# Performance work log

Measured on AMD Instinct MI355X. Metric: run time of the kernel, lower is better.

## Reference

```python
import jax, jax.numpy as jnp
import numpy as np
from jax import lax

B, C, H, W = 4, 64, 256, 256
CH = C // 2  # attention hidden channels


def conv2d_same(x, w, b):
    # x: [B,Ci,H,W], w: [Co,Ci,kh,kw]
    y = lax.conv_general_dilated(x, w, (1, 1), 'SAME',
                                 dimension_numbers=('NCHW', 'OIHW', 'NCHW'))
    return y + b[None, :, None, None]


def conv1x1(x, w):
    # w: [Co,Ci]
    return jnp.einsum('oi,bihw->bohw', w, x)


def irnn_scan(x, w, b, axis, reverse):
    """Directional IRNN: h_t = relu(x_t + w_c * h_{t-1} + b_c), per channel.
    axis: 2 (rows/H) or 3 (cols/W). reverse=True scans from the far edge
    (e.g. bottom-to-top for 'up', right-to-left for 'left')."""
    xs = jnp.moveaxis(x, axis, 0)            # [L, B, C, rest]
    wb = w[None, :, None]                    # broadcast over [B, C, rest]
    bb = b[None, :, None]

    def step(h, xt):
        h = jax.nn.relu(xt + wb * h + bb)
        return h, h

    h0 = jnp.zeros_like(xs[0])
    _, ys = lax.scan(step, h0, xs, reverse=reverse)
    return jnp.moveaxis(ys, 0, axis)


def setup_inputs() -> dict:
    key = jax.random.key(0)
    ks = jax.random.split(key, 16)
    d = {}
    d['x'] = jax.random.normal(ks[0], (B, C, H, W), dtype=jnp.float32)
    # conv_in: 1x1, no bias
    d['w_in'] = jax.random.normal(ks[1], (C, C), dtype=jnp.float32) * 0.05
    # IRNN depthwise 1x1 weights (init alpha=1.0 in torch) + biases
    for i, name in enumerate(['up', 'right', 'down', 'left']):
        d['w_' + name] = jnp.ones((C,), dtype=jnp.float32)
        d['b_' + name] = jax.random.normal(ks[2 + i], (C,), dtype=jnp.float32) * 0.01
    # convD2: 1x1, 4C -> C, no bias
    d['wD2'] = jax.random.normal(ks[6], (C, 4 * C), dtype=jnp.float32) * 0.01
    # attention layers
    d['a1_w'] = jax.random.normal(ks[7], (CH, C, 3, 3), dtype=jnp.float32) * 0.05
    d['a1_b'] = jnp.zeros((CH,), dtype=jnp.float32)
    d['a2_w'] = jax.random.normal(ks[8], (CH, CH, 3, 3), dtype=jnp.float32) * 0.05
    d['a2_b'] = jnp.zeros((CH,), dtype=jnp.float32)
    d['a3_w'] = jax.random.normal(ks[9], (1, CH), dtype=jnp.float32) * 0.05
    d['a3_b'] = jnp.zeros((1,), dtype=jnp.float32)
    return d


def reference(x, w_in, w_up, b_up, w_right, b_right, w_down, b_down,
              w_left, b_left, wD2, a1_w, a1_b, a2_w, a2_b, a3_w, a3_b):
    out = conv1x1(x, w_in)
    # four directional spatial IRNN scans
    top_up = irnn_scan(out, w_up, b_up, axis=2, reverse=True)     # bottom->top
    top_right = irnn_scan(out, w_right, b_right, axis=3, reverse=False)  # left->right
    top_down = irnn_scan(out, w_down, b_down, axis=2, reverse=False)     # top->bottom
    top_left = irnn_scan(out, w_left, b_left, axis=3, reverse=True)      # right->left
    cat = jnp.concatenate([top_up, top_right, top_down, top_left], axis=1)  # [B,4C,H,W]
    out = jax.nn.relu(conv1x1(cat, wD2))
    # attention gate
    a = jax.nn.relu(conv2d_same(out, a1_w, a1_b))
    a = jax.nn.relu(conv2d_same(a, a2_w, a2_b))
    a = conv1x1(a, a3_w) + a3_b[None, :, None, None]
    weight = jax.nn.sigmoid(a)                # [B,1,H,W]
    return jax.nn.relu(x * weight)
```

## Files before the change

kernel.cpp:

```cpp
#include <hip/hip_runtime.h>
#include <hip/hip_bf16.h>

#define HWSZ  65536

typedef unsigned short ushort_t;
typedef unsigned int   uint_t;
typedef __attribute__((ext_vector_type(8))) _Float16 half8;
typedef __attribute__((ext_vector_type(4))) float f32x4;

static __device__ __forceinline__ void gl_lds16(const void* g, void* l) {
    __builtin_amdgcn_global_load_lds(
        (const __attribute__((address_space(1))) unsigned int*)g,
        (__attribute__((address_space(3))) unsigned int*)l, 16, 0, 0);
}

__global__ __launch_bounds__(256) void k1_mfma(
    const float* __restrict__ x, const float* __restrict__ w_in,
    _Float16* __restrict__ out0)
{
    __shared__ float xs[64][64];
    int b   = blockIdx.x >> 10;
    int hw0 = (blockIdx.x & 1023) << 6;
    const float* xb = x + ((size_t)b * 64) * HWSZ + hw0;
    int wave = threadIdx.x >> 6, lane = threadIdx.x & 63;
    int n16 = lane & 15, quad = lane >> 4;

    for (int idx = threadIdx.x; idx < 1024; idx += 256) {
        int i = idx >> 4, p4 = (idx & 15) << 2;
        *(float4*)&xs[i][p4] = *(const float4*)(xb + (size_t)i * HWSZ + p4);
    }

    half8 Bh[2], Bl[2];
#pragma unroll
    for (int s = 0; s < 2; s++) {
        const float* wp = w_in + (wave * 16 + n16) * 64 + s * 32 + quad * 8;
#pragma unroll
        for (int j = 0; j < 8; j++) {
            float v = wp[j];
            _Float16 h = (_Float16)v;
            float r = v - (float)h;
            Bh[s][j] = h; Bl[s][j] = (_Float16)r;
        }
    }
    __syncthreads();

    f32x4 acc[4] = {};
#pragma unroll
    for (int j = 0; j < 4; j++) {
#pragma unroll
        for (int s = 0; s < 2; s++) {
            half8 Ah, Al;
#pragma unroll
            for (int jj = 0; jj < 8; jj++) {
                float v = xs[s * 32 + quad * 8 + jj][j * 16 + n16];
                _Float16 h = (_Float16)v;
                float r = v - (float)h;
                Ah[jj] = h; Al[jj] = (_Float16)r;
            }
            acc[j] = __builtin_amdgcn_mfma_f32_16x16x32_f16(Ah, Bh[s], acc[j], 0, 0, 0);
            acc[j] = __builtin_amdgcn_mfma_f32_16x16x32_f16(Al, Bh[s], acc[j], 0, 0, 0);
            acc[j] = __builtin_amdgcn_mfma_f32_16x16x32_f16(Ah, Bl[s], acc[j], 0, 0, 0);
        }
    }
    _Float16* ob = out0 + ((size_t)b * HWSZ + hw0) * 64 + wave * 16;
#pragma unroll
    for (int j = 0; j < 4; j++)
#pragma unroll
        for (int r = 0; r < 4; r++) {
            int px = j * 16 + quad * 4 + r;
            ob[(size_t)px * 64 + n16] = (_Float16)acc[j][r];
        }
}

__global__ __launch_bounds__(256) void k2_scan(
    const _Float16* __restrict__ out0,
    const float* __restrict__ w_up, const float* __restrict__ b_up,
    const float* __restrict__ w_rt, const float* __restrict__ b_rt,
    const float* __restrict__ w_dn, const float* __restrict__ b_dn,
    const float* __restrict__ w_lf, const float* __restrict__ b_lf,
    _Float16* __restrict__ cat)
{
    int c = threadIdx.x & 63;
    int q = threadIdx.x >> 6;
    bool vert = blockIdx.x < 256;
    int bid = blockIdx.x & 255;
    int b = bid >> 6, g = bid & 63;
    int line = g * 4 + q;
    size_t base = (size_t)b * HWSZ;

    float w0v, b0v, w1v, b1v; int coff0, coff1;
    if (vert) { w0v = w_dn[c]; b0v = b_dn[c]; coff0 = 128;
                w1v = w_up[c]; b1v = b_up[c]; coff1 = 0; }
    else      { w0v = w_rt[c]; b0v = b_rt[c]; coff0 = 64;
                w1v = w_lf[c]; b1v = b_lf[c]; coff1 = 192; }

#pragma unroll
    for (int pass = 0; pass < 2; pass++) {
        float wv = pass ? w1v : w0v, bv = pass ? b1v : b0v;
        int coff = pass ? coff1 : coff0;
        float h = 0.f;
        for (int k0 = 0; k0 < 256; k0 += 8) {
            float v[8];
#pragma unroll
            for (int jx = 0; jx < 8; jx++) {
                int i = pass ? 255 - (k0 + jx) : (k0 + jx);
                size_t pix = vert ? (base + i * 256 + line) : (base + line * 256 + i);
                v[jx] = (float)out0[pix * 64 + c];
            }
#pragma unroll
            for (int jx = 0; jx < 8; jx++) {
                int i = pass ? 255 - (k0 + jx) : (k0 + jx);
                size_t pix = vert ? (base + i * 256 + line) : (base + line * 256 + i);
                h = fmaxf(0.f, v[jx] + wv * h + bv);
                cat[pix * 256 + coff + c] = (_Float16)h;
            }
        }
    }
}

__global__ __launch_bounds__(256) void packall(
    const float* __restrict__ wD2, const float* __restrict__ a1w,
    const float* __restrict__ a2w,
    _Float16* __restrict__ wf, _Float16* __restrict__ p1,
    _Float16* __restrict__ p2)
{
    int i = blockIdx.x * 256 + threadIdx.x;
    if (i < 16384) {
        wf[i] = (_Float16)wD2[i];
        return;
    }
    int k = i - 16384;
    if (k < 18432) {
        int j = k & 7, lane = (k >> 3) & 63, st = k >> 9;
        int s = st >> 1, t = st & 1;
        int oc = t * 16 + (lane & 15);
        int gk = s * 32 + (lane >> 4) * 8 + j;
        int dydx = gk >> 6, ic = gk & 63;
        p1[k] = (_Float16)a1w[((oc * 64 + ic) * 3 + dydx / 3) * 3 + dydx % 3];
    } else if (k < 27648) {
        int e = k - 18432;
        int j = e & 7, lane = (e >> 3) & 63, st = e >> 9;
        int s = st >> 1, t = st & 1;
        int oc = t * 16 + (lane & 15);
        int gk = s * 32 + (lane >> 4) * 8 + j;
        int dydx = gk >> 5, ic = gk & 31;
        p2[e] = (_Float16)a2w[((oc * 32 + ic) * 3 + dydx / 3) * 3 + dydx % 3];
    }
}

__global__ __launch_bounds__(256) void k3_mfma(
    const _Float16* __restrict__ cat, const _Float16* __restrict__ wf,
    _Float16* __restrict__ out3)
{
    __shared__ _Float16 As[64 * 256];
    int wave = threadIdx.x >> 6, lane = threadIdx.x & 63;
    int n16 = lane & 15, quad = lane >> 4;
    size_t p0 = (size_t)blockIdx.x * 64;

    half8 B[8];
#pragma unroll
    for (int s = 0; s < 8; s++)
        B[s] = *(const half8*)(wf + (size_t)(wave * 16 + n16) * 256 + s * 32 + quad * 8);

#pragma unroll
    for (int it = 0; it < 8; it++) {
        int px = wave * 16 + it * 2 + (lane >> 5);
        int pu = lane & 31;
        int lu = pu ^ (px & 7);
        const _Float16* gp = cat + ((p0 + px) << 8) + lu * 8;
        _Float16* lp = As + wave * 4096 + it * 512;
        gl_lds16(gp, lp);
    }
    __syncthreads();

    f32x4 acc[4] = {};
#pragma unroll
    for (int j = 0; j < 4; j++) {
        int px = j * 16 + n16;
        const _Float16* lrow = As + px * 256;
        int x7 = px & 7;
#pragma unroll
        for (int s = 0; s < 8; s++) {
            int phys = (s * 4 + quad) ^ x7;
            half8 a = *(const half8*)(lrow + phys * 8);
            acc[j] = __builtin_amdgcn_mfma_f32_16x16x32_f16(a, B[s], acc[j], 0, 0, 0);
        }
    }

#pragma unroll
    for (int j = 0; j < 4; j++)
#pragma unroll
        for (int r = 0; r < 4; r++) {
            size_t op = (p0 + j * 16 + quad * 4 + r) * 64 + wave * 16 + n16;
            out3[op] = (_Float16)fmaxf(acc[j][r], 0.f);
        }
}

template <int IC>
__global__ __launch_bounds__(256) void convmfma(
    const _Float16* __restrict__ in, const _Float16* __restrict__ pb,
    const float* __restrict__ bias, _Float16* __restrict__ oh)
{
    constexpr int UPX = IC / 8;
    constexpr int KST = IC / 32;
    constexpr int PPS = 64 / UPX;
    __shared__ _Float16 Ls[6 * 66 * IC];

    int wave = threadIdx.x >> 6, lane = threadIdx.x & 63;
    int n16 = lane & 15, quad = lane >> 4;
    int bid = blockIdx.x;
    int bb  = bid >> 8;
    int hh0 = ((bid >> 2) & 63) << 2;
    int w0  = (bid & 3) << 6;
    const _Float16* ib = in + (size_t)bb * HWSZ * IC;

#pragma unroll
    for (int it = 0; it < (6 * UPX) / 4; it++) {
        int q   = it * 4 + wave;
        int r   = q / UPX, seg = q % UPX;
        int gh  = hh0 - 1 + r;
        int pxr = seg * PPS + lane / UPX;
        int pu  = lane % UPX;
        int px_lin = r * 66 + 1 + pxr;
        int lu  = (UPX == 8) ? (pu ^ (px_lin & 7)) : pu;
        _Float16* lp = Ls + (size_t)(r * 66 + 1 + seg * PPS) * IC;
        if ((unsigned)gh < 256u) {
            const _Float16* gp = ib + ((size_t)(gh * 256 + w0 + pxr)) * IC + lu * 8;
            gl_lds16(gp, lp);
        } else {
            half8 z = {};
            *(half8*)(lp + (size_t)lane * 8) = z;
        }
    }
    if (threadIdx.x < 12 * UPX) {
        int pu = threadIdx.x % UPX;
        int ph = threadIdx.x / UPX;
        int r = ph >> 1, side = ph & 1;
        int col = side ? 65 : 0;
        int gh = hh0 - 1 + r;
        int gw = w0 - 1 + side * 65;
        int px_lin = r * 66 + col;
        int lu = (UPX == 8) ? (pu ^ (px_lin & 7)) : pu;
        half8 v = {};
        if ((unsigned)gh < 256u && (unsigned)gw < 256u)
            v = *(const half8*)(ib + ((size_t)(gh * 256 + gw)) * IC + lu * 8);
        *(half8*)(Ls + (size_t)px_lin * IC + pu * 8) = v;
    }
    __syncthreads();

    f32x4 acc[4][2] = {};
#pragma unroll
    for (int dydx = 0; dydx < 9; dydx++) {
        int dy = dydx / 3, dx = dydx % 3;
        int r_lds = wave + dy;
#pragma unroll
        for (int kst = 0; kst < KST; kst++) {
            int s = dydx * KST + kst;
            half8 B0 = *(const half8*)(pb + (size_t)((s * 2 + 0) * 64 + lane) * 8);
            half8 B1 = *(const half8*)(pb + (size_t)((s * 2 + 1) * 64 + lane) * 8);
            int u = kst * 4 + quad;
#pragma unroll
            for (int j = 0; j < 4; j++) {
                int px_lin = r_lds * 66 + j * 16 + n16 + dx;
                int phys = (UPX == 8) ? (u ^ (px_lin & 7)) : u;
                half8 A = *(const half8*)(Ls + (size_t)px_lin * IC + phys * 8);
                acc[j][0] = __builtin_amdgcn_mfma_f32_16x16x32_f16(A, B0, acc[j][0], 0, 0, 0);
                acc[j][1] = __builtin_amdgcn_mfma_f32_16x16x32_f16(A, B1, acc[j][1], 0, 0, 0);
            }
        }
    }

    int hh = hh0 + wave;
#pragma unroll
    for (int t = 0; t < 2; t++) {
        float bv = bias[t * 16 + n16];
#pragma unroll
        for (int j = 0; j < 4; j++)
#pragma unroll
            for (int r = 0; r < 4; r++) {
                int wp = w0 + j * 16 + quad * 4 + r;
                size_t op = ((size_t)bb * HWSZ + hh * 256 + wp) * 32 + t * 16 + n16;
                oh[op] = (_Float16)fmaxf(acc[j][t][r] + bv, 0.f);
            }
    }
}

__global__ __launch_bounds__(256) void k6_gate(
    const _Float16* __restrict__ a2, const float* __restrict__ a3w,
    const float* __restrict__ a3b, const float* __restrict__ x,
    float* __restrict__ out)
{
    int pix = blockIdx.x * 256 + threadIdx.x;
    int b = pix >> 16;
    int hw = pix & 65535;
    const _Float16* ap = a2 + (size_t)pix * 32;
    half8 q0 = *(const half8*)(ap);
    half8 q1 = *(const half8*)(ap + 8);
    half8 q2 = *(const half8*)(ap + 16);
    half8 q3 = *(const half8*)(ap + 24);
    float s = a3b[0];
#pragma unroll
    for (int j = 0; j < 8; j++) {
        s += a3w[j]      * (float)q0[j];
        s += a3w[j + 8]  * (float)q1[j];
        s += a3w[j + 16] * (float)q2[j];
        s += a3w[j + 24] * (float)q3[j];
    }
    float g = 1.f / (1.f + __expf(-s));
    const float* xb = x + (size_t)b * 64 * HWSZ + hw;
    float* ob = out + (size_t)b * 64 * HWSZ + hw;
#pragma unroll 8
    for (int c = 0; c < 64; c++)
        ob[(size_t)c * HWSZ] = fmaxf(0.f, xb[(size_t)c * HWSZ] * g);
}

extern "C" void kernel_launch(void* const* d_in, const int* in_sizes, int n_in,
                              void* d_out, int out_size, void* d_ws, size_t ws_size,
                              hipStream_t stream)
{
    const float* x     = (const float*)d_in[0];
    const float* w_in  = (const float*)d_in[1];
    const float* w_up  = (const float*)d_in[2];
    const float* b_up  = (const float*)d_in[3];
    const float* w_rt  = (const float*)d_in[4];
    const float* b_rt  = (const float*)d_in[5];
    const float* w_dn  = (const float*)d_in[6];
    const float* b_dn  = (const float*)d_in[7];
    const float* w_lf  = (const float*)d_in[8];
    const float* b_lf  = (const float*)d_in[9];
    const float* wD2   = (const float*)d_in[10];
    const float* a1w   = (const float*)d_in[11];
    const float* a1b   = (const float*)d_in[12];
    const float* a2w   = (const float*)d_in[13];
    const float* a2b   = (const float*)d_in[14];
    const float* a3w   = (const float*)d_in[15];
    const float* a3b   = (const float*)d_in[16];
    float* out = (float*)d_out;

    char* ws = (char*)d_ws;
    _Float16* out0 = (_Float16*)ws;
    _Float16* out3 = (_Float16*)ws;
    _Float16* wf16 = (_Float16*)(ws + (33ull << 20));
    _Float16* p1   = (_Float16*)(ws + (34ull << 20));
    _Float16* p2   = (_Float16*)(ws + (35ull << 20));
    _Float16* cat  = (_Float16*)(ws + (64ull << 20));
    _Float16* a1   = (_Float16*)(ws + (64ull << 20));
    _Float16* a2   = (_Float16*)(ws + (80ull << 20));

    k1_mfma   <<<4096, 256, 0, stream>>>(x, w_in, out0);
    k2_scan   <<<512,  256, 0, stream>>>(out0, w_up, b_up, w_rt, b_rt,
                                         w_dn, b_dn, w_lf, b_lf, cat);
    packall   <<<172,  256, 0, stream>>>(wD2, a1w, a2w, wf16, p1, p2);
    k3_mfma   <<<4096, 256, 0, stream>>>(cat, wf16, out3);
    convmfma<64><<<1024, 256, 0, stream>>>(out3, p1, a1b, a1);
    convmfma<32><<<1024, 256, 0, stream>>>(a1, p2, a2b, a2);
    k6_gate   <<<1024, 256, 0, stream>>>(a2, a3w, a3b, x, out);
}
```

Before: 271.1 us.

## Split IRNN scan directions across blocks and precompute fp16 hi/lo splits in LDS

The scan kernel now launches one block per direction instead of running two sequential passes per block. The grid doubles to 1024 blocks and each thread's serial chain is half as long. Separately, the 1x1 input conv now converts each fp32 value into an fp16 high/low pair once into padded LDS tiles. The MFMA loop then reads these with vector loads, so the conversion is no longer repeated per wave. The cost is extra LDS and one more barrier in k1.

```diff
diff --git a/kernel.cpp b/kernel.cpp
--- a/kernel.cpp
+++ b/kernel.cpp
@@ -19,6 +19,8 @@
     _Float16* __restrict__ out0)
 {
     __shared__ float xs[64][64];
+    __shared__ _Float16 ah[64][72];
+    __shared__ _Float16 al[64][72];
     int b   = blockIdx.x >> 10;
     int hw0 = (blockIdx.x & 1023) << 6;
     const float* xb = x + ((size_t)b * 64) * HWSZ + hw0;
@@ -44,19 +46,37 @@
     }
     __syncthreads();
 
+    {
+        int px  = threadIdx.x >> 2;
+        int ic0 = (threadIdx.x & 3) << 4;
+        half8 h0, h1, l0, l1;
+#pragma unroll
+        for (int e = 0; e < 8; e++) {
+            float v = xs[ic0 + e][px];
+            _Float16 h = (_Float16)v;
+            h0[e] = h; l0[e] = (_Float16)(v - (float)h);
+        }
+#pragma unroll
+        for (int e = 0; e < 8; e++) {
+            float v = xs[ic0 + 8 + e][px];
+            _Float16 h = (_Float16)v;
+            h1[e] = h; l1[e] = (_Float16)(v - (float)h);
+        }
+        *(half8*)&ah[px][ic0]     = h0;
+        *(half8*)&ah[px][ic0 + 8] = h1;
+        *(half8*)&al[px][ic0]     = l0;
+        *(half8*)&al[px][ic0 + 8] = l1;
+    }
+    __syncthreads();
+
     f32x4 acc[4] = {};
 #pragma unroll
     for (int j = 0; j < 4; j++) {
+        int px = j * 16 + n16;
 #pragma unroll
         for (int s = 0; s < 2; s++) {
-            half8 Ah, Al;
-#pragma unroll
-            for (int jj = 0; jj < 8; jj++) {
-                float v = xs[s * 32 + quad * 8 + jj][j * 16 + n16];
-                _Float16 h = (_Float16)v;
-                float r = v - (float)h;
-                Ah[jj] = h; Al[jj] = (_Float16)r;
-            }
+            half8 Ah = *(const half8*)&ah[px][s * 32 + quad * 8];
+            half8 Al = *(const half8*)&al[px][s * 32 + quad * 8];
             acc[j] = __builtin_amdgcn_mfma_f32_16x16x32_f16(Ah, Bh[s], acc[j], 0, 0, 0);
             acc[j] = __builtin_amdgcn_mfma_f32_16x16x32_f16(Al, Bh[s], acc[j], 0, 0, 0);
             acc[j] = __builtin_amdgcn_mfma_f32_16x16x32_f16(Ah, Bl[s], acc[j], 0, 0, 0);
@@ -82,38 +102,36 @@
 {
     int c = threadIdx.x & 63;
     int q = threadIdx.x >> 6;
-    bool vert = blockIdx.x < 256;
+    int dir = blockIdx.x >> 8;
     int bid = blockIdx.x & 255;
     int b = bid >> 6, g = bid & 63;
     int line = g * 4 + q;
     size_t base = (size_t)b * HWSZ;
-
-    float w0v, b0v, w1v, b1v; int coff0, coff1;
-    if (vert) { w0v = w_dn[c]; b0v = b_dn[c]; coff0 = 128;
-                w1v = w_up[c]; b1v = b_up[c]; coff1 = 0; }
-    else      { w0v = w_rt[c]; b0v = b_rt[c]; coff0 = 64;
-                w1v = w_lf[c]; b1v = b_lf[c]; coff1 = 192; }
-
-#pragma unroll
-    for (int pass = 0; pass < 2; pass++) {
-        float wv = pass ? w1v : w0v, bv = pass ? b1v : b0v;
-        int coff = pass ? coff1 : coff0;
-        float h = 0.f;
-        for (int k0 = 0; k0 < 256; k0 += 8) {
-            float v[8];
-#pragma unroll
-            for (int jx = 0; jx < 8; jx++) {
-                int i = pass ? 255 - (k0 + jx) : (k0 + jx);
-                size_t pix = vert ? (base + i * 256 + line) : (base + line * 256 + i);
-                v[jx] = (float)out0[pix * 64 + c];
-            }
-#pragma unroll
-            for (int jx = 0; jx < 8; jx++) {
-                int i = pass ? 255 - (k0 + jx) : (k0 + jx);
-                size_t pix = vert ? (base + i * 256 + line) : (base + line * 256 + i);
-                h = fmaxf(0.f, v[jx] + wv * h + bv);
-                cat[pix * 256 + coff + c] = (_Float16)h;
-            }
+    bool vert = dir < 2;
+    bool rev  = dir & 1;
+
+    const float *wp, *bp; int coff;
+    if      (dir == 0) { wp = w_dn; bp = b_dn; coff = 128; }
+    else if (dir == 1) { wp = w_up; bp = b_up; coff = 0;   }
+    else if (dir == 2) { wp = w_rt; bp = b_rt; coff = 64;  }
+    else               { wp = w_lf; bp = b_lf; coff = 192; }
+    float wv = wp[c], bv = bp[c];
+
+    float h = 0.f;
+    for (int k0 = 0; k0 < 256; k0 += 8) {
+        float v[8];
+#pragma unroll
+        for (int jx = 0; jx < 8; jx++) {
+            int i = rev ? 255 - (k0 + jx) : (k0 + jx);
+            size_t pix = vert ? (base + i * 256 + line) : (base + line * 256 + i);
+            v[jx] = (float)out0[pix * 64 + c];
+        }
+#pragma unroll
+        for (int jx = 0; jx < 8; jx++) {
+            int i = rev ? 255 - (k0 + jx) : (k0 + jx);
+            size_t pix = vert ? (base + i * 256 + line) : (base + line * 256 + i);
+            h = fmaxf(0.f, v[jx] + wv * h + bv);
+            cat[pix * 256 + coff + c] = (_Float16)h;
         }
     }
 }
@@ -348,7 +366,7 @@
     _Float16* a2   = (_Float16*)(ws + (80ull << 20));
 
     k1_mfma   <<<4096, 256, 0, stream>>>(x, w_in, out0);
-    k2_scan   <<<512,  256, 0, stream>>>(out0, w_up, b_up, w_rt, b_rt,
+    k2_scan   <<<1024, 256, 0, stream>>>(out0, w_up, b_up, w_rt, b_rt,
                                          w_dn, b_dn, w_lf, b_lf, cat);
     packall   <<<172,  256, 0, stream>>>(wD2, a1w, a2w, wf16, p1, p2);
     k3_mfma   <<<4096, 256, 0, stream>>>(cat, wf16, out3);
```

Result: no change. 270.4 us (-0.2%).
